# Kernel tuning notes

Measured on AMD Instinct MI355X. Metric: run time of the kernel, lower is better.

## Reference

```python
import jax, jax.numpy as jnp
import numpy as np

N, CIN, H, W_ = 16, 64, 56, 56
COUT, K, STRIDE, PAD = 64, 3, 1, 1


def setup_inputs() -> dict:
    key = jax.random.key(0)
    k1, k2 = jax.random.split(key)
    x = jax.random.normal(k1, (N, CIN, H, W_), dtype=jnp.float32)
    adder = jax.random.normal(k2, (COUT, CIN, K, K), dtype=jnp.float32)
    return {"x": x, "adder": adder}


def reference(x, adder):
    # AdderNet 2d: out[n,co,h,w] = -sum_{ci,kh,kw} |patch(n,:,h,w) - adder[co]|
    n, c, h, w = x.shape
    co = adder.shape[0]
    # im2col: [N, C*K*K, Ho, Wo]; feature dim ordered (c, kh, kw), matching
    # torch.nn.functional.unfold and adder.reshape(Co, C*K*K).
    patches = jax.lax.conv_general_dilated_patches(
        x, filter_shape=(K, K), window_strides=(STRIDE, STRIDE),
        padding=((PAD, PAD), (PAD, PAD)))
    n_, ckk, ho, wo = patches.shape
    p = patches.reshape(n_, ckk, ho * wo)          # [N, CKK, L]
    w_col = adder.reshape(co, ckk)                 # [Co, CKK]

    def per_filter(wf):
        # wf: [CKK]; negative L1 distance of this filter to every patch
        return -jnp.sum(jnp.abs(p - wf[None, :, None]), axis=1)  # [N, L]

    # Sequential map over output channels avoids materializing the full
    # [Co, N, CKK, L] broadcast tensor (~7 GB); peak extra memory is one
    # [N, CKK, L] diff buffer per step.
    out = jax.lax.map(per_filter, w_col)           # [Co, N, L]
    out = out.transpose(1, 0, 2).reshape(n_, co, ho, wo)
    return out
```

## Files before the change

### kernel.cpp

```cpp
#include <hip/hip_runtime.h>

#define N_    16
#define CIN_  64
#define HW_   56
#define COUT_ 64
#define HPR   58
#define WST   60
#define PLANE (HPR * WST)
#define PLANE_PAD 3584

__global__ void pad_x_kernel(const float* __restrict__ x, float* __restrict__ xp) {
    int idx = blockIdx.x * 256 + threadIdx.x;
    const int total = N_ * CIN_ * PLANE_PAD;
    if (idx >= total) return;
    int rem = idx % PLANE_PAD;
    int nc  = idx / PLANE_PAD;
    int h   = rem / WST;
    int w   = rem % WST;
    float v = 0.f;
    if (h >= 1 && h <= HW_ && w >= 1 && w <= HW_)
        v = x[((size_t)nc * HW_ + (h - 1)) * HW_ + (w - 1)];
    xp[idx] = v;
}

__global__ __launch_bounds__(256, 2) void adder_main_kernel(
    const float* __restrict__ xp, const float* __restrict__ wt,
    float* __restrict__ out) {
    __shared__ float lds[2][2][PLANE_PAD];

    const int bid  = blockIdx.x;
    const int n    = bid >> 5;
    const int cop  = bid & 31;
    const int tid  = threadIdx.x;
    const int wid  = tid >> 6;
    const int lane = tid & 63;
    const int coidx  = wid >> 1;
    const int cihalf = wid & 1;
    const int co   = cop * 2 + coidx;
    const int tx = lane & 7, ty = lane >> 3;
    const int h0 = ty * 7, w0 = tx * 7;

    const int sgH = wid >> 1;
    const int sgW = wid & 1;
    const size_t gplane0 = (size_t)(n * CIN_) * PLANE_PAD;

    #define STAGEP(bufi, ci_) { \
        const float* gsrc_ = xp + gplane0 + (size_t)(sgH * 32 + (ci_)) * PLANE_PAD; \
        float* ldst_ = &lds[bufi][sgH][0]; \
        _Pragma("unroll") \
        for (int k_ = 0; k_ < 7; ++k_) { \
            int ch_ = k_ * 2 + sgW; \
            __builtin_amdgcn_global_load_lds( \
                (const __attribute__((address_space(1))) void*)(gsrc_ + ch_ * 256 + lane * 4), \
                (__attribute__((address_space(3))) void*)(ldst_ + ch_ * 256), 16, 0, 0); \
        } }

    float acc[7][7] = {};
    const int rb = h0 * WST + w0;

    STAGEP(0, 0)
    __syncthreads();

    for (int it = 0; it < 32; ++it) {
        const int cur = it & 1;
        if (it < 31) STAGEP(cur ^ 1, it + 1)

        const float* lp = &lds[cur][cihalf][0];
        const int ci = cihalf * 32 + it;
        const float* wp = wt + (size_t)co * 576 + (size_t)ci * 9;
        float w9[9];
        #pragma unroll
        for (int k = 0; k < 9; ++k) w9[k] = wp[k];

        float buf[9][9];
        #define LROW(r) { _Pragma("unroll") \
            for (int c = 0; c < 9; ++c) buf[r][c] = lp[rb + (r) * WST + c]; }
        #define CROW(oh) { _Pragma("unroll") \
            for (int kh = 0; kh < 3; ++kh) { \
                _Pragma("unroll") \
                for (int kw = 0; kw < 3; ++kw) { \
                    float wv = w9[kh * 3 + kw]; \
                    _Pragma("unroll") \
                    for (int j = 0; j < 7; ++j) \
                        acc[oh][j] += fabsf(buf[(oh) + kh][j + kw] - wv); \
                } } }

        LROW(0) LROW(1) LROW(2) LROW(3)
        CROW(0) LROW(4)
        CROW(1) LROW(5)
        CROW(2) LROW(6)
        CROW(3) LROW(7)
        CROW(4) LROW(8)
        CROW(5)
        CROW(6)
        #undef LROW
        #undef CROW

        __syncthreads();
    }

    float* red = &lds[0][0][0];
    if (cihalf == 1) {
        float* rp = red + (size_t)(coidx * 64 + lane) * 49;
        #pragma unroll
        for (int oh = 0; oh < 7; ++oh)
            #pragma unroll
            for (int j = 0; j < 7; ++j) rp[oh * 7 + j] = acc[oh][j];
    }
    __syncthreads();
    if (cihalf == 0) {
        const float* rp = red + (size_t)(coidx * 64 + lane) * 49;
        float* ob = out + (((size_t)(n * COUT_ + co)) * HW_ + h0) * HW_ + w0;
        #pragma unroll
        for (int oh = 0; oh < 7; ++oh)
            #pragma unroll
            for (int j = 0; j < 7; ++j)
                ob[oh * HW_ + j] = -(acc[oh][j] + rp[oh * 7 + j]);
    }
    #undef STAGEP
}

extern "C" void kernel_launch(void* const* d_in, const int* in_sizes, int n_in,
                              void* d_out, int out_size, void* d_ws, size_t ws_size,
                              hipStream_t stream) {
    const float* x     = (const float*)d_in[0];
    const float* adder = (const float*)d_in[1];
    float* out = (float*)d_out;

    float* xp = (float*)d_ws;

    const int padTotal = N_ * CIN_ * PLANE_PAD;
    pad_x_kernel<<<(padTotal + 255) / 256, 256, 0, stream>>>(x, xp);
    adder_main_kernel<<<N_ * 32, 256, 0, stream>>>(xp, adder, out);
}
```

Measured before the change: 200.1 us.

## Split input channels across blocks and reduce partial sums with global atomics

Each block now handles four output channels over a 16-channel slice of the input, with one wave per output channel sharing a single staged input plane. This replaces the in-block two-way channel split and its LDS reduction. The change doubles the grid, halves LDS per block and raises the occupancy hint, all aimed at using more CUs and hiding latency. It adds a memset of the output plus four-way float atomicAdd contention per output element, and the summation order becomes nondeterministic.

```diff
diff --git a/kernel.cpp b/kernel.cpp
--- a/kernel.cpp
+++ b/kernel.cpp
@@ -6,7 +6,6 @@
 #define COUT_ 64
 #define HPR   58
 #define WST   60
-#define PLANE (HPR * WST)
 #define PLANE_PAD 3584
 
 __global__ void pad_x_kernel(const float* __restrict__ x, float* __restrict__ xp) {
@@ -23,58 +22,55 @@
     xp[idx] = v;
 }
 
-__global__ __launch_bounds__(256, 2) void adder_main_kernel(
+__global__ __launch_bounds__(256, 4) void adder_main_kernel(
     const float* __restrict__ xp, const float* __restrict__ wt,
     float* __restrict__ out) {
-    __shared__ float lds[2][2][PLANE_PAD];
+    __shared__ float lds[2][PLANE_PAD];
 
-    const int bid  = blockIdx.x;
-    const int n    = bid >> 5;
-    const int cop  = bid & 31;
-    const int tid  = threadIdx.x;
-    const int wid  = tid >> 6;
-    const int lane = tid & 63;
-    const int coidx  = wid >> 1;
-    const int cihalf = wid & 1;
-    const int co   = cop * 2 + coidx;
+    const int bid   = blockIdx.x;
+    const int n     = bid >> 6;
+    const int quad  = (bid >> 2) & 15;
+    const int chunk = bid & 3;
+    const int tid   = threadIdx.x;
+    const int wid   = tid >> 6;
+    const int lane  = tid & 63;
+    const int co    = quad * 4 + wid;
+    const int ci0   = chunk * 16;
     const int tx = lane & 7, ty = lane >> 3;
     const int h0 = ty * 7, w0 = tx * 7;
+    const int rb = h0 * WST + w0;
 
-    const int sgH = wid >> 1;
-    const int sgW = wid & 1;
-    const size_t gplane0 = (size_t)(n * CIN_) * PLANE_PAD;
+    const float* gplane = xp + (size_t)(n * CIN_ + ci0) * PLANE_PAD;
+    const float* wbase  = wt + (size_t)co * 576 + (size_t)ci0 * 9;
 
-    #define STAGEP(bufi, ci_) { \
-        const float* gsrc_ = xp + gplane0 + (size_t)(sgH * 32 + (ci_)) * PLANE_PAD; \
-        float* ldst_ = &lds[bufi][sgH][0]; \
+    #define STAGEP(bufi, i_) { \
+        const float* gsrc_ = gplane + (size_t)(i_) * PLANE_PAD; \
         _Pragma("unroll") \
-        for (int k_ = 0; k_ < 7; ++k_) { \
-            int ch_ = k_ * 2 + sgW; \
-            __builtin_amdgcn_global_load_lds( \
-                (const __attribute__((address_space(1))) void*)(gsrc_ + ch_ * 256 + lane * 4), \
-                (__attribute__((address_space(3))) void*)(ldst_ + ch_ * 256), 16, 0, 0); \
+        for (int k_ = 0; k_ < 4; ++k_) { \
+            int c_ = wid + 4 * k_; \
+            if (c_ < 14) \
+                __builtin_amdgcn_global_load_lds( \
+                    (const __attribute__((address_space(1))) void*)(gsrc_ + c_ * 256 + lane * 4), \
+                    (__attribute__((address_space(3))) void*)(&lds[bufi][c_ * 256]), 16, 0, 0); \
         } }
 
     float acc[7][7] = {};
-    const int rb = h0 * WST + w0;
 
     STAGEP(0, 0)
     __syncthreads();
 
-    for (int it = 0; it < 32; ++it) {
+    for (int it = 0; it < 16; ++it) {
         const int cur = it & 1;
-        if (it < 31) STAGEP(cur ^ 1, it + 1)
+        if (it < 15) STAGEP(cur ^ 1, it + 1)
 
-        const float* lp = &lds[cur][cihalf][0];
-        const int ci = cihalf * 32 + it;
-        const float* wp = wt + (size_t)co * 576 + (size_t)ci * 9;
+        const float* wp = wbase + it * 9;
         float w9[9];
         #pragma unroll
         for (int k = 0; k < 9; ++k) w9[k] = wp[k];
 
         float buf[9][9];
         #define LROW(r) { _Pragma("unroll") \
-            for (int c = 0; c < 9; ++c) buf[r][c] = lp[rb + (r) * WST + c]; }
+            for (int c = 0; c < 9; ++c) buf[r][c] = lds[cur][rb + (r) * WST + c]; }
         #define CROW(oh) { _Pragma("unroll") \
             for (int kh = 0; kh < 3; ++kh) { \
                 _Pragma("unroll") \
@@ -99,24 +95,12 @@
         __syncthreads();
     }
 
-    float* red = &lds[0][0][0];
-    if (cihalf == 1) {
-        float* rp = red + (size_t)(coidx * 64 + lane) * 49;
+    float* ob = out + (((size_t)(n * COUT_ + co)) * HW_ + h0) * HW_ + w0;
+    #pragma unroll
+    for (int oh = 0; oh < 7; ++oh)
         #pragma unroll
-        for (int oh = 0; oh < 7; ++oh)
-            #pragma unroll
-            for (int j = 0; j < 7; ++j) rp[oh * 7 + j] = acc[oh][j];
-    }
-    __syncthreads();
-    if (cihalf == 0) {
-        const float* rp = red + (size_t)(coidx * 64 + lane) * 49;
-        float* ob = out + (((size_t)(n * COUT_ + co)) * HW_ + h0) * HW_ + w0;
-        #pragma unroll
-        for (int oh = 0; oh < 7; ++oh)
-            #pragma unroll
-            for (int j = 0; j < 7; ++j)
-                ob[oh * HW_ + j] = -(acc[oh][j] + rp[oh * 7 + j]);
-    }
+        for (int j = 0; j < 7; ++j)
+            atomicAdd(&ob[oh * HW_ + j], -acc[oh][j]);
     #undef STAGEP
 }
 
@@ -129,7 +113,8 @@
 
     float* xp = (float*)d_ws;
 
+    hipMemsetAsync(d_out, 0, (size_t)out_size * sizeof(float), stream);
     const int padTotal = N_ * CIN_ * PLANE_PAD;
     pad_x_kernel<<<(padTotal + 255) / 256, 256, 0, stream>>>(x, xp);
-    adder_main_kernel<<<N_ * 32, 256, 0, stream>>>(xp, adder, out);
+    adder_main_kernel<<<N_ * 64, 256, 0, stream>>>(xp, adder, out);
 }
```

New measurement: 746.1 us. +272.9%, slower.
